# Kernel optimization log

Measured on AMD Instinct MI355X. Metric: run time of the kernel, lower is better.

## Reference

```python
import jax, jax.numpy as jnp
import numpy as np

D_POINTS, D_MODEL, K, B, N = 64, 128, 16, 2, 16384


def _linear(x, w, b=None):
    y = x @ w.T
    return y if b is None else y + b


def setup_inputs() -> dict:
    key = jax.random.key(0)
    ks = jax.random.split(key, 16)
    s = 0.02
    inp = {
        "new_xyz": jax.random.normal(ks[0], (B, N, 3), jnp.float32),
        "grouped_xyz": jax.random.normal(ks[1], (B, 3, N, K), jnp.float32),
        "grouped_idx": jax.random.randint(ks[2], (B, N, K), 0, N),
        "features": jax.random.normal(ks[3], (B, N, D_POINTS), jnp.float32),
        "fc1_w": jax.random.normal(ks[4], (D_MODEL, D_POINTS), jnp.float32) * s,
        "fc1_b": jnp.zeros((D_MODEL,), jnp.float32),
        "wq": jax.random.normal(ks[5], (D_MODEL, D_MODEL), jnp.float32) * s,
        "wk": jax.random.normal(ks[6], (D_MODEL, D_MODEL), jnp.float32) * s,
        "wv": jax.random.normal(ks[7], (D_MODEL, D_MODEL), jnp.float32) * s,
        "delta_w1": jax.random.normal(ks[8], (D_MODEL, 3), jnp.float32) * s,
        "delta_b1": jnp.zeros((D_MODEL,), jnp.float32),
        "delta_w2": jax.random.normal(ks[9], (D_MODEL, D_MODEL), jnp.float32) * s,
        "delta_b2": jnp.zeros((D_MODEL,), jnp.float32),
        "gamma_w1": jax.random.normal(ks[10], (D_MODEL, D_MODEL), jnp.float32) * s,
        "gamma_b1": jnp.zeros((D_MODEL,), jnp.float32),
        "gamma_w2": jax.random.normal(ks[11], (D_MODEL, D_MODEL), jnp.float32) * s,
        "gamma_b2": jnp.zeros((D_MODEL,), jnp.float32),
    }
    return inp


def reference(new_xyz, grouped_xyz, grouped_idx, features,
              fc1_w, fc1_b, wq, wk, wv,
              delta_w1, delta_b1, delta_w2, delta_b2,
              gamma_w1, gamma_b1, gamma_w2, gamma_b2):
    # x: [B,N,d_model]
    x = _linear(features, fc1_w, fc1_b)
    q = x @ wq.T                               # [B,N,d]
    kx = x @ wk.T                              # [B,N,d]
    vx = x @ wv.T                              # [B,N,d]
    gather = jax.vmap(lambda a, i: a[i])       # per-batch gather -> [B,N,K,d]
    k = gather(kx, grouped_idx)
    v = gather(vx, grouped_idx)
    # pos_enc: fc_delta(new_xyz[:,:,None] - grouped_xyz.permute(0,2,3,1))
    rel = new_xyz[:, :, None, :] - jnp.transpose(grouped_xyz, (0, 2, 3, 1))  # [B,N,K,3]
    pos_enc = _linear(jax.nn.relu(_linear(rel, delta_w1, delta_b1)), delta_w2, delta_b2)
    # attn: fc_gamma(q - k + pos_enc), softmax over neighbor axis
    h = q[:, :, None, :] - k + pos_enc
    attn = _linear(jax.nn.relu(_linear(h, gamma_w1, gamma_b1)), gamma_w2, gamma_b2)
    attn = jax.nn.softmax(attn / np.sqrt(D_MODEL).astype(np.float32), axis=-2)
    out = jnp.einsum('bmnf,bmnf->bmf', attn, v + pos_enc)
    return out
```

## Files before the change

### kernel.cpp

```cpp
#include <hip/hip_runtime.h>
#include <math.h>

#define BB   2
#define NPTS 16384
#define KNB  16
#define DPTS 64
#define DM   128

typedef float  f32x4  __attribute__((ext_vector_type(4)));
typedef short  bf16x8 __attribute__((ext_vector_type(8)));

__device__ __forceinline__ unsigned short f2bf(float f) {
    union { float f; unsigned u; } v; v.f = f;
    unsigned r = v.u + 0x7FFFu + ((v.u >> 16) & 1u);
    return (unsigned short)(r >> 16);
}
__device__ __forceinline__ float bf2f(unsigned short h) {
    union { unsigned u; float f; } v; v.u = ((unsigned)h) << 16;
    return v.f;
}

#define WOFF_DW2  0
#define WOFF_GW1  16384
#define WOFF_GW2  32768
#define WOFF_WQ   49152
#define WOFF_WK   65536
#define WOFF_WV   81920
#define WOFF_FC1  98304
#define WTOT      106496

__global__ __launch_bounds__(256) void cvtw_kernel(
    const float* __restrict__ dw2, const float* __restrict__ gw1,
    const float* __restrict__ gw2, const float* __restrict__ wq,
    const float* __restrict__ wk, const float* __restrict__ wv,
    const float* __restrict__ fc1_w, unsigned short* __restrict__ wb)
{
    const int i = blockIdx.x * 256 + threadIdx.x;
    if (i >= WTOT) return;
    float v;
    if (i < WOFF_WQ) {
        const int which = i >> 14, off = i & 16383;
        v = (which == 0) ? dw2[off] : (which == 1) ? gw1[off] : gw2[off];
    } else if (i < WOFF_FC1) {
        const int j = i - WOFF_WQ;
        const int which = j >> 14, off = j & 16383;
        v = (which == 0) ? wq[off] : (which == 1) ? wk[off] : wv[off];
    } else {
        v = fc1_w[i - WOFF_FC1];
    }
    wb[i] = f2bf(v);
}

#define ABSTR 136

__device__ __forceinline__ void mfma_gemm(const unsigned short* __restrict__ AB,
                                          const unsigned short* __restrict__ Wb,
                                          int lane, int wbase, f32x4 acc[4][2])
{
    const int c = lane & 15, g = lane >> 4;
    bf16x8 Bf[2][4];
#pragma unroll
    for (int ct = 0; ct < 2; ++ct)
#pragma unroll
        for (int ks = 0; ks < 4; ++ks)
            Bf[ct][ks] = *(const bf16x8*)&Wb[(wbase + ct * 16 + c) * DM + ks * 32 + g * 8];
#pragma unroll
    for (int rt = 0; rt < 4; ++rt) {
        bf16x8 Af[4];
#pragma unroll
        for (int ks = 0; ks < 4; ++ks)
            Af[ks] = *(const bf16x8*)&AB[(rt * 16 + c) * ABSTR + ks * 32 + g * 8];
#pragma unroll
        for (int ct = 0; ct < 2; ++ct)
#pragma unroll
            for (int ks = 0; ks < 4; ++ks)
                acc[rt][ct] = __builtin_amdgcn_mfma_f32_16x16x32_bf16(
                    Af[ks], Bf[ct][ks], acc[rt][ct], 0, 0, 0);
    }
}

#define P_MT  64
#define FSTR  72

__global__ __launch_bounds__(256, 4) void proj_kernel(
    const float* __restrict__ features, const float* __restrict__ fc1_b,
    const unsigned short* __restrict__ wbf,
    unsigned short* __restrict__ qws, unsigned short* __restrict__ kws,
    unsigned short* __restrict__ vws)
{
    __shared__ __align__(16) unsigned short FB[P_MT * FSTR];
    __shared__ __align__(16) unsigned short XB[P_MT * ABSTR];

    const int tid  = threadIdx.x;
    const int lane = tid & 63;
    const int wave = tid >> 6;
    const int wbase = wave * 32;
    const int c  = lane & 15;
    const int g  = lane >> 4;
    const int g4 = g * 4;
    const size_t gp0 = (size_t)blockIdx.x * P_MT;

    for (int i = tid; i < P_MT * 8; i += 256) {
        const int r = i >> 3, o = i & 7;
        const float4 a = *(const float4*)&features[(gp0 + r) * DPTS + o * 8];
        const float4 b = *(const float4*)&features[(gp0 + r) * DPTS + o * 8 + 4];
        bf16x8 t;
        t[0] = (short)f2bf(a.x); t[1] = (short)f2bf(a.y);
        t[2] = (short)f2bf(a.z); t[3] = (short)f2bf(a.w);
        t[4] = (short)f2bf(b.x); t[5] = (short)f2bf(b.y);
        t[6] = (short)f2bf(b.z); t[7] = (short)f2bf(b.w);
        *(bf16x8*)&FB[r * FSTR + o * 8] = t;
    }
    __syncthreads();

    {
        const unsigned short* fw = wbf + WOFF_FC1;
        f32x4 acc[4][2];
#pragma unroll
        for (int rt = 0; rt < 4; ++rt)
#pragma unroll
            for (int ct = 0; ct < 2; ++ct) acc[rt][ct] = (f32x4)0.f;
        bf16x8 Bf[2][2];
#pragma unroll
        for (int ct = 0; ct < 2; ++ct)
#pragma unroll
            for (int ks = 0; ks < 2; ++ks)
                Bf[ct][ks] = *(const bf16x8*)&fw[(wbase + ct * 16 + c) * DPTS + ks * 32 + g * 8];
#pragma unroll
        for (int rt = 0; rt < 4; ++rt) {
            bf16x8 Af[2];
#pragma unroll
            for (int ks = 0; ks < 2; ++ks)
                Af[ks] = *(const bf16x8*)&FB[(rt * 16 + c) * FSTR + ks * 32 + g * 8];
#pragma unroll
            for (int ct = 0; ct < 2; ++ct)
#pragma unroll
                for (int ks = 0; ks < 2; ++ks)
                    acc[rt][ct] = __builtin_amdgcn_mfma_f32_16x16x32_bf16(
                        Af[ks], Bf[ct][ks], acc[rt][ct], 0, 0, 0);
        }
#pragma unroll
        for (int ct = 0; ct < 2; ++ct) {
            const int col = wbase + ct * 16 + c;
            const float bb = fc1_b[col];
#pragma unroll
            for (int rt = 0; rt < 4; ++rt)
#pragma unroll
                for (int rg = 0; rg < 4; ++rg)
                    XB[(rt * 16 + g4 + rg) * ABSTR + col] = f2bf(acc[rt][ct][rg] + bb);
        }
    }
    __syncthreads();

    const unsigned short* wmat[3] = { wbf + WOFF_WQ, wbf + WOFF_WK, wbf + WOFF_WV };
    unsigned short* outp[3] = { qws, kws, vws };
#pragma unroll
    for (int m = 0; m < 3; ++m) {
        f32x4 acc[4][2];
#pragma unroll
        for (int rt = 0; rt < 4; ++rt)
#pragma unroll
            for (int ct = 0; ct < 2; ++ct) acc[rt][ct] = (f32x4)0.f;
        mfma_gemm(XB, wmat[m], lane, wbase, acc);
#pragma unroll
        for (int ct = 0; ct < 2; ++ct) {
            const int col = wbase + ct * 16 + c;
#pragma unroll
            for (int rt = 0; rt < 4; ++rt)
#pragma unroll
                for (int rg = 0; rg < 4; ++rg)
                    outp[m][(gp0 + rt * 16 + g4 + rg) * DM + col] = f2bf(acc[rt][ct][rg]);
        }
    }
}

#define K2_PTS 4
#define K2_R   (K2_PTS * KNB)

__global__ __launch_bounds__(256, 4) void attn_kernel(
    const float* __restrict__ new_xyz, const float* __restrict__ grouped_xyz,
    const int* __restrict__ grouped_idx,
    const float* __restrict__ dw1, const float* __restrict__ db1,
    const float* __restrict__ db2,
    const float* __restrict__ gb1, const float* __restrict__ gb2,
    const unsigned short* __restrict__ wbf,
    const unsigned short* __restrict__ qws, const unsigned short* __restrict__ kws,
    const unsigned short* __restrict__ vws,
    float* __restrict__ out)
{
    __shared__ __align__(16) unsigned short AB[K2_R * ABSTR];
    __shared__ __align__(16) unsigned short POSL[K2_R * ABSTR];
    __shared__ float REL[K2_R * 3];
    __shared__ int   IDX[K2_R];

    const int tid  = threadIdx.x;
    const int lane = tid & 63;
    const int wave = tid >> 6;
    const int wbase = wave * 32;
    const int c  = lane & 15;
    const int g  = lane >> 4;
    const int g4 = g * 4;
    const int rr = tid >> 4;
    const int o8 = (tid & 15) * 8;

    const int b   = blockIdx.x / (NPTS / K2_PTS);
    const int m0  = (blockIdx.x % (NPTS / K2_PTS)) * K2_PTS;
    const size_t gp0 = (size_t)b * NPTS + m0;
    const size_t bN  = (size_t)b * NPTS;
    const float inv_sqrt_d = 0.08838834764831845f;

    const unsigned short* dw2b = wbf + WOFF_DW2;
    const unsigned short* gw1b = wbf + WOFF_GW1;
    const unsigned short* gw2b = wbf + WOFF_GW2;

    float wr[24], bbv[8];
    {
        const float4* wsrc = (const float4*)&dw1[o8 * 3];
#pragma unroll
        for (int t = 0; t < 6; ++t) ((float4*)wr)[t] = wsrc[t];
        const float4* bsrc = (const float4*)&db1[o8];
        ((float4*)bbv)[0] = bsrc[0];
        ((float4*)bbv)[1] = bsrc[1];
    }

    if (tid < K2_R) {
        const int p = tid >> 4, j = tid & 15;
        const size_t m = gp0 + p;
        const int mi = m0 + p;
        IDX[tid] = grouped_idx[m * KNB + j];
#pragma unroll
        for (int cc = 0; cc < 3; ++cc)
            REL[tid * 3 + cc] = new_xyz[m * 3 + cc]
                              - grouped_xyz[(((size_t)b * 3 + cc) * NPTS + mi) * KNB + j];
    }
    __syncthreads();

#pragma unroll
    for (int it = 0; it < 4; ++it) {
        const int r = it * 16 + rr;
        const float rx = REL[r * 3 + 0], ry = REL[r * 3 + 1], rz = REL[r * 3 + 2];
        bf16x8 t;
#pragma unroll
        for (int j = 0; j < 8; ++j) {
            float v = bbv[j];
            v = fmaf(rx, wr[j * 3 + 0], v);
            v = fmaf(ry, wr[j * 3 + 1], v);
            v = fmaf(rz, wr[j * 3 + 2], v);
            t[j] = (short)f2bf(fmaxf(v, 0.f));
        }
        *(bf16x8*)&AB[r * ABSTR + o8] = t;
    }
    __syncthreads();

    f32x4 posr[4][2];
    {
#pragma unroll
        for (int rt = 0; rt < 4; ++rt)
#pragma unroll
            for (int ct = 0; ct < 2; ++ct) posr[rt][ct] = (f32x4)0.f;
        mfma_gemm(AB, dw2b, lane, wbase, posr);
#pragma unroll
        for (int ct = 0; ct < 2; ++ct) {
            const int col = wbase + ct * 16 + c;
            const float bb = db2[col];
#pragma unroll
            for (int rt = 0; rt < 4; ++rt)
#pragma unroll
                for (int rg = 0; rg < 4; ++rg) {
                    posr[rt][ct][rg] += bb;
                    POSL[(rt * 16 + g4 + rg) * ABSTR + col] = f2bf(posr[rt][ct][rg]);
                }
        }
    }
    __syncthreads();

#pragma unroll
    for (int it = 0; it < 4; ++it) {
        const int r = it * 16 + rr;
        const bf16x8 q8 = *(const bf16x8*)&qws[(gp0 + it) * DM + o8];
        const bf16x8 k8 = *(const bf16x8*)&kws[(bN + IDX[r]) * DM + o8];
        const bf16x8 p8 = *(const bf16x8*)&POSL[r * ABSTR + o8];
        bf16x8 t;
#pragma unroll
        for (int j = 0; j < 8; ++j) {
            const float hv = bf2f((unsigned short)q8[j])
                           - bf2f((unsigned short)k8[j])
                           + bf2f((unsigned short)p8[j]);
            t[j] = (short)f2bf(hv);
        }
        *(bf16x8*)&AB[r * ABSTR + o8] = t;
    }
    __syncthreads();

    {
        f32x4 acc[4][2];
#pragma unroll
        for (int rt = 0; rt < 4; ++rt)
#pragma unroll
            for (int ct = 0; ct < 2; ++ct) acc[rt][ct] = (f32x4)0.f;
        mfma_gemm(AB, gw1b, lane, wbase, acc);
        __syncthreads();
#pragma unroll
        for (int ct = 0; ct < 2; ++ct) {
            const int col = wbase + ct * 16 + c;
            const float bb = gb1[col];
#pragma unroll
            for (int rt = 0; rt < 4; ++rt)
#pragma unroll
                for (int rg = 0; rg < 4; ++rg)
                    AB[(rt * 16 + g4 + rg) * ABSTR + col] = f2bf(fmaxf(acc[rt][ct][rg] + bb, 0.f));
        }
    }
    __syncthreads();

    f32x4 lg[4][2];
#pragma unroll
    for (int rt = 0; rt < 4; ++rt)
#pragma unroll
        for (int ct = 0; ct < 2; ++ct) lg[rt][ct] = (f32x4)0.f;
    mfma_gemm(AB, gw2b, lane, wbase, lg);
#pragma unroll
    for (int ct = 0; ct < 2; ++ct) {
        const int col = wbase + ct * 16 + c;
        const float bb = gb2[col];
#pragma unroll
        for (int rt = 0; rt < 4; ++rt)
#pragma unroll
            for (int rg = 0; rg < 4; ++rg)
                lg[rt][ct][rg] = (lg[rt][ct][rg] + bb) * inv_sqrt_d;
    }

#pragma unroll
    for (int rt = 0; rt < 4; ++rt)
#pragma unroll
    for (int ct = 0; ct < 2; ++ct) {
        const int col = wbase + ct * 16 + c;
        f32x4 l = lg[rt][ct];
        float mx = fmaxf(fmaxf(l[0], l[1]), fmaxf(l[2], l[3]));
        mx = fmaxf(mx, __shfl_xor(mx, 16));
        mx = fmaxf(mx, __shfl_xor(mx, 32));
        f32x4 e;
        e[0] = __expf(l[0] - mx); e[1] = __expf(l[1] - mx);
        e[2] = __expf(l[2] - mx); e[3] = __expf(l[3] - mx);
        float s = e[0] + e[1] + e[2] + e[3];
        s += __shfl_xor(s, 16);
        s += __shfl_xor(s, 32);
        float o = 0.f;
#pragma unroll
        for (int rg = 0; rg < 4; ++rg) {
            const int row = rt * 16 + g4 + rg;
            const float vv = bf2f(vws[(bN + IDX[row]) * DM + col]) + posr[rt][ct][rg];
            o = fmaf(e[rg], vv, o);
        }
        o += __shfl_xor(o, 16);
        o += __shfl_xor(o, 32);
        if (g == 0)
            out[(gp0 + rt) * DM + col] = o / s;
    }
}

extern "C" void kernel_launch(void* const* d_in, const int* in_sizes, int n_in,
                              void* d_out, int out_size, void* d_ws, size_t ws_size,
                              hipStream_t stream)
{
    const float* new_xyz     = (const float*)d_in[0];
    const float* grouped_xyz = (const float*)d_in[1];
    const int*   grouped_idx = (const int*)d_in[2];
    const float* features    = (const float*)d_in[3];
    const float* fc1_w = (const float*)d_in[4];
    const float* fc1_b = (const float*)d_in[5];
    const float* wq    = (const float*)d_in[6];
    const float* wk    = (const float*)d_in[7];
    const float* wv    = (const float*)d_in[8];
    const float* dw1   = (const float*)d_in[9];
    const float* db1   = (const float*)d_in[10];
    const float* dw2   = (const float*)d_in[11];
    const float* db2   = (const float*)d_in[12];
    const float* gw1   = (const float*)d_in[13];
    const float* gb1   = (const float*)d_in[14];
    const float* gw2   = (const float*)d_in[15];
    const float* gb2   = (const float*)d_in[16];
    float* out = (float*)d_out;

    unsigned short* ws = (unsigned short*)d_ws;
    const size_t npt = (size_t)BB * NPTS * DM;
    unsigned short* qws = ws;
    unsigned short* kws = ws + npt;
    unsigned short* vws = ws + 2 * npt;
    unsigned short* wbf = ws + 3 * npt;

    cvtw_kernel<<<(WTOT + 255) / 256, 256, 0, stream>>>(
        dw2, gw1, gw2, wq, wk, wv, fc1_w, wbf);

    proj_kernel<<<(BB * NPTS) / P_MT, 256, 0, stream>>>(
        features, fc1_b, wbf, qws, kws, vws);

    attn_kernel<<<(BB * NPTS) / K2_PTS, 256, 0, stream>>>(
        new_xyz, grouped_xyz, grouped_idx,
        dw1, db1, db2, gb1, gb2,
        wbf, qws, kws, vws, out);
}
```

Baseline: 175.3 us.

## Prefetch q/k gathers early, double-buffer LDS to drop a barrier, use exp2/rcp

Moves the q and gathered-k global loads to the start of the attention kernel, so their latency overlaps the positional-encoding MLP instead of stalling later. The gamma hidden activations are written to a second LDS buffer, which was the positional buffer and is renamed SB. That removes one __syncthreads between the first gamma GEMM and its write-back. The softmax now folds log2(e) into the scale and uses hardware exp2 and a reciprocal instead of a division, and the bf16 conversion switches to the library intrinsic. Holding the prefetched loads raises register pressure and may lower occupancy, and the approximate rcp slightly changes numerics.

```diff
diff --git a/kernel.cpp b/kernel.cpp
--- a/kernel.cpp
+++ b/kernel.cpp
@@ -1,4 +1,5 @@
 #include <hip/hip_runtime.h>
+#include <hip/hip_bf16.h>
 #include <math.h>
 
 #define BB   2
@@ -11,9 +12,9 @@
 typedef short  bf16x8 __attribute__((ext_vector_type(8)));
 
 __device__ __forceinline__ unsigned short f2bf(float f) {
-    union { float f; unsigned u; } v; v.f = f;
-    unsigned r = v.u + 0x7FFFu + ((v.u >> 16) & 1u);
-    return (unsigned short)(r >> 16);
+    union { __hip_bfloat16 h; unsigned short u; } v;
+    v.h = __float2bfloat16(f);
+    return v.u;
 }
 __device__ __forceinline__ float bf2f(unsigned short h) {
     union { unsigned u; float f; } v; v.u = ((unsigned)h) << 16;
@@ -189,7 +190,7 @@
     float* __restrict__ out)
 {
     __shared__ __align__(16) unsigned short AB[K2_R * ABSTR];
-    __shared__ __align__(16) unsigned short POSL[K2_R * ABSTR];
+    __shared__ __align__(16) unsigned short SB[K2_R * ABSTR];
     __shared__ float REL[K2_R * 3];
     __shared__ int   IDX[K2_R];
 
@@ -207,7 +208,7 @@
     const int m0  = (blockIdx.x % (NPTS / K2_PTS)) * K2_PTS;
     const size_t gp0 = (size_t)b * NPTS + m0;
     const size_t bN  = (size_t)b * NPTS;
-    const float inv_sqrt_d = 0.08838834764831845f;
+    const float SCL = 0.12751743342f;
 
     const unsigned short* dw2b = wbf + WOFF_DW2;
     const unsigned short* gw1b = wbf + WOFF_GW1;
@@ -234,6 +235,14 @@
                               - grouped_xyz[(((size_t)b * 3 + cc) * NPTS + mi) * KNB + j];
     }
     __syncthreads();
+
+    bf16x8 q8[4], k8[4];
+#pragma unroll
+    for (int it = 0; it < 4; ++it) {
+        const int r = it * 16 + rr;
+        q8[it] = *(const bf16x8*)&qws[(gp0 + it) * DM + o8];
+        k8[it] = *(const bf16x8*)&kws[(bN + IDX[r]) * DM + o8];
+    }
 
 #pragma unroll
     for (int it = 0; it < 4; ++it) {
@@ -268,7 +277,7 @@
 #pragma unroll
                 for (int rg = 0; rg < 4; ++rg) {
                     posr[rt][ct][rg] += bb;
-                    POSL[(rt * 16 + g4 + rg) * ABSTR + col] = f2bf(posr[rt][ct][rg]);
+                    SB[(rt * 16 + g4 + rg) * ABSTR + col] = f2bf(posr[rt][ct][rg]);
                 }
         }
     }
@@ -277,14 +286,12 @@
 #pragma unroll
     for (int it = 0; it < 4; ++it) {
         const int r = it * 16 + rr;
-        const bf16x8 q8 = *(const bf16x8*)&qws[(gp0 + it) * DM + o8];
-        const bf16x8 k8 = *(const bf16x8*)&kws[(bN + IDX[r]) * DM + o8];
-        const bf16x8 p8 = *(const bf16x8*)&POSL[r * ABSTR + o8];
+        const bf16x8 p8 = *(const bf16x8*)&SB[r * ABSTR + o8];
         bf16x8 t;
 #pragma unroll
         for (int j = 0; j < 8; ++j) {
-            const float hv = bf2f((unsigned short)q8[j])
-                           - bf2f((unsigned short)k8[j])
+            const float hv = bf2f((unsigned short)q8[it][j])
+                           - bf2f((unsigned short)k8[it][j])
                            + bf2f((unsigned short)p8[j]);
             t[j] = (short)f2bf(hv);
         }
@@ -299,7 +306,6 @@
 #pragma unroll
             for (int ct = 0; ct < 2; ++ct) acc[rt][ct] = (f32x4)0.f;
         mfma_gemm(AB, gw1b, lane, wbase, acc);
-        __syncthreads();
 #pragma unroll
         for (int ct = 0; ct < 2; ++ct) {
             const int col = wbase + ct * 16 + c;
@@ -308,7 +314,7 @@
             for (int rt = 0; rt < 4; ++rt)
 #pragma unroll
                 for (int rg = 0; rg < 4; ++rg)
-                    AB[(rt * 16 + g4 + rg) * ABSTR + col] = f2bf(fmaxf(acc[rt][ct][rg] + bb, 0.f));
+                    SB[(rt * 16 + g4 + rg) * ABSTR + col] = f2bf(fmaxf(acc[rt][ct][rg] + bb, 0.f));
         }
     }
     __syncthreads();
@@ -318,7 +324,7 @@
     for (int rt = 0; rt < 4; ++rt)
 #pragma unroll
         for (int ct = 0; ct < 2; ++ct) lg[rt][ct] = (f32x4)0.f;
-    mfma_gemm(AB, gw2b, lane, wbase, lg);
+    mfma_gemm(SB, gw2b, lane, wbase, lg);
 #pragma unroll
     for (int ct = 0; ct < 2; ++ct) {
         const int col = wbase + ct * 16 + c;
@@ -327,7 +333,7 @@
         for (int rt = 0; rt < 4; ++rt)
 #pragma unroll
             for (int rg = 0; rg < 4; ++rg)
-                lg[rt][ct][rg] = (lg[rt][ct][rg] + bb) * inv_sqrt_d;
+                lg[rt][ct][rg] = (lg[rt][ct][rg] + bb) * SCL;
     }
 
 #pragma unroll
@@ -340,8 +346,10 @@
         mx = fmaxf(mx, __shfl_xor(mx, 16));
         mx = fmaxf(mx, __shfl_xor(mx, 32));
         f32x4 e;
-        e[0] = __expf(l[0] - mx); e[1] = __expf(l[1] - mx);
-        e[2] = __expf(l[2] - mx); e[3] = __expf(l[3] - mx);
+        e[0] = __builtin_amdgcn_exp2f(l[0] - mx);
+        e[1] = __builtin_amdgcn_exp2f(l[1] - mx);
+        e[2] = __builtin_amdgcn_exp2f(l[2] - mx);
+        e[3] = __builtin_amdgcn_exp2f(l[3] - mx);
         float s = e[0] + e[1] + e[2] + e[3];
         s += __shfl_xor(s, 16);
         s += __shfl_xor(s, 32);
@@ -355,7 +363,7 @@
         o += __shfl_xor(o, 16);
         o += __shfl_xor(o, 32);
         if (g == 0)
-            out[(gp0 + rt) * DM + col] = o / s;
+            out[(gp0 + rt) * DM + col] = o * __builtin_amdgcn_rcpf(s);
     }
 }
 
```

New measurement: 167.0 us. 4.7% less time.
